# Kernel tuning notes

Hardware: AMD Instinct MI355X
Metric: run time of the kernel (lower is better)

The kernel has to match this reference:

```python
import jax, jax.numpy as jnp
import numpy as np
from jax import lax

B = 128

# ---- 4-qubit statevector helpers (RY + CNOT circuit is real-valued) ----

def _init_state(n):
    s = jnp.zeros((n, 2, 2, 2, 2), jnp.float32)
    return s.at[:, 0, 0, 0, 0].set(1.0)


def _ry(state, theta, wire):
    # RY(t) = [[cos t/2, -sin t/2],[sin t/2, cos t/2]]; theta: scalar or [N]
    s = jnp.moveaxis(state, wire + 1, 1)
    c = jnp.cos(theta * 0.5)
    sn = jnp.sin(theta * 0.5)
    if jnp.ndim(theta) > 0:
        c = c.reshape(-1, 1, 1, 1)
        sn = sn.reshape(-1, 1, 1, 1)
    a, b = s[:, 0], s[:, 1]
    s = jnp.stack([c * a - sn * b, sn * a + c * b], axis=1)
    return jnp.moveaxis(s, 1, wire + 1)


def _cnot(state, ctrl, tgt):
    s = jnp.moveaxis(state, [ctrl + 1, tgt + 1], [1, 2])
    s = jnp.concatenate([s[:, :1], jnp.flip(s[:, 1:], axis=2)], axis=1)
    return jnp.moveaxis(s, [1, 2], [ctrl + 1, tgt + 1])


def _random_layer(state, thetas):
    for i in range(4):
        state = _ry(state, thetas[i], i)
        state = _cnot(state, i, (i + 1) % 4)
    return state


def _measure_z(state, wire):
    p = jnp.moveaxis(state, wire + 1, 1) ** 2
    p = p.reshape(p.shape[0], 2, -1).sum(-1)
    return p[:, 0] - p[:, 1]


def setup_inputs() -> dict:
    key = jax.random.key(0)
    ks = jax.random.split(key, 12)

    def n(k, shape, scale):
        return jax.random.normal(k, shape, jnp.float32) * scale

    return {
        "x": jax.random.normal(ks[0], (B, 3, 249, 249), jnp.float32),
        "conv1_w": n(ks[1], (6, 3, 5, 5), 0.1),
        "conv1_b": jnp.zeros((6,), jnp.float32),
        "conv2_w": n(ks[2], (15, 6, 3, 3), 0.1),
        "conv2_b": jnp.zeros((15,), jnp.float32),
        "fc1_w": n(ks[3], (120, 55815), 1.0 / np.sqrt(55815.0)),
        "fc1_b": jnp.zeros((120,), jnp.float32),
        "fc2_w": n(ks[4], (84, 120), 1.0 / np.sqrt(120.0)),
        "fc2_b": jnp.zeros((84,), jnp.float32),
        "fc3_w": n(ks[5], (1, 84), 1.0 / np.sqrt(84.0)),
        "fc3_b": jnp.zeros((1,), jnp.float32),
        "head_thetas": jax.random.uniform(ks[6], (4,), jnp.float32, 0.0, 2.0 * np.pi),
        "qf_thetas": jax.random.uniform(ks[7], (4,), jnp.float32, 0.0, 2.0 * np.pi),
        "lin_w": n(ks[8], (1, 784), 1.0 / np.sqrt(784.0)),
        "lin_b": jnp.zeros((1,), jnp.float32),
    }


def reference(x, conv1_w, conv1_b, conv2_w, conv2_b, fc1_w, fc1_b, fc2_w, fc2_b,
              fc3_w, fc3_b, head_thetas, qf_thetas, lin_w, lin_b):
    bsz = x.shape[0]

    def conv(y, w, b, stride):
        y = lax.conv_general_dilated(y, w, (stride, stride), [(1, 1), (1, 1)],
                                     dimension_numbers=("NCHW", "OIHW", "NCHW"))
        return y + b[None, :, None, None]

    def pool(y):  # MaxPool2d(kernel=2, stride=1)
        return lax.reduce_window(y, -jnp.inf, lax.max, (1, 1, 2, 2), (1, 1, 1, 1), "VALID")

    # ---- conv branch (dropout = identity in eval) ----
    h = pool(jax.nn.relu(conv(x, conv1_w, conv1_b, 2)))          # [B,6,123,123]
    h = pool(jax.nn.relu(conv(h, conv2_w, conv2_b, 2)))          # [B,15,61,61]
    h = h.reshape(bsz, -1)                                        # [B,55815]
    h = jax.nn.relu(h @ fc1_w.T + fc1_b)
    h = jax.nn.relu(h @ fc2_w.T + fc2_b)
    logit = (h @ fc3_w.T + fc3_b)[:, 0]                           # [B]
    st = _init_state(bsz)
    st = _ry(st, logit, 0)
    st = _random_layer(st, head_thetas)
    probs_conv = jax.nn.sigmoid(_measure_z(st, 0))[:, None]       # [B,1]

    # ---- quanvolution branch ----
    gray = x.mean(axis=1, keepdims=True)                          # [B,1,249,249]
    g = jax.image.resize(gray, (bsz, 1, 28, 28), method="linear")[:, 0]
    # 2x2 patches, row-major, element order [tl, tr, bl, br]
    patches = g.reshape(bsz, 14, 2, 14, 2).transpose(0, 1, 3, 2, 4).reshape(bsz * 196, 4)
    st = _init_state(bsz * 196)
    for w in range(4):
        st = _ry(st, patches[:, w], w)
    st = _random_layer(st, qf_thetas)
    feats = jnp.stack([_measure_z(st, w) for w in range(4)], axis=1).reshape(bsz, 784)
    probs_q = jax.nn.sigmoid(feats @ lin_w.T + lin_b)             # [B,1]

    probs = (probs_conv + probs_q) * 0.5
    return jnp.concatenate([probs, 1.0 - probs], axis=-1)         # [B,2]
```

## Files before the change

### kernel.cpp

```cpp
#include <hip/hip_runtime.h>
#include <math.h>

#define DEV static __device__ __forceinline__

template <int W>
DEV void q_ry(float s[16], float th) {
  float c = cosf(th * 0.5f), sn = sinf(th * 0.5f);
  constexpr int m = 8 >> W;
#pragma unroll
  for (int i = 0; i < 16; ++i) {
    if (!(i & m)) {
      float a = s[i], b = s[i | m];
      s[i] = c * a - sn * b;
      s[i | m] = sn * a + c * b;
    }
  }
}
template <int C, int T>
DEV void q_cnot(float s[16]) {
  constexpr int mc = 8 >> C, mt = 8 >> T;
#pragma unroll
  for (int i = 0; i < 16; ++i) {
    if ((i & mc) && !(i & mt)) {
      float t = s[i]; s[i] = s[i | mt]; s[i | mt] = t;
    }
  }
}
template <int W>
DEV float q_mz(const float s[16]) {
  constexpr int m = 8 >> W;
  float p = 0.f;
#pragma unroll
  for (int i = 0; i < 16; ++i) p += (i & m) ? -s[i] * s[i] : s[i] * s[i];
  return p;
}
DEV void q_layer(float s[16], const float* __restrict__ th) {
  q_ry<0>(s, th[0]); q_cnot<0, 1>(s);
  q_ry<1>(s, th[1]); q_cnot<1, 2>(s);
  q_ry<2>(s, th[2]); q_cnot<2, 3>(s);
  q_ry<3>(s, th[3]); q_cnot<3, 0>(s);
}

__global__ void k_wre(const float* __restrict__ c1w, float* __restrict__ wre1) {
  int t = blockIdx.x * 256 + threadIdx.x;
  if (t < 450) {
    int g = t / 30, rem = t % 30;
    int ci = g / 5, ky = g % 5, kx = rem / 6, co = rem % 6;
    wre1[t] = c1w[co * 75 + ci * 25 + ky * 5 + kx];
  }
}

DEV int c1_rowbase(int row) { return row * 39 + ((row >> 1) & 1); }

__global__ __launch_bounds__(256, 4) void k_conv1(const float* __restrict__ x,
                                                  const float* __restrict__ wre1,
                                                  const float* __restrict__ bia,
                                                  float* __restrict__ out) {
  __shared__ float smem[6800];
  float (*ct)[42][19] = (float (*)[42][19])smem;
  int b = blockIdx.z;
  int PY0 = blockIdx.y * 41, PX0 = blockIdx.x * 16;
  int iy0 = PY0 * 2 - 1, ix0 = PX0 * 2 - 1;
  int tid = threadIdx.x;
  const float* xb = x + (size_t)b * 186003;
  int r = tid / 6, seg = tid - 6 * (tid / 6);
  float acc[6][3];
#pragma unroll
  for (int co = 0; co < 6; ++co) {
    float bv = bia[co];
#pragma unroll
    for (int c = 0; c < 3; ++c) acc[co][c] = bv;
  }
  {
    const float* xci = xb;
#pragma unroll
    for (int s = 0; s < 14; ++s) {
      int idx = s * 256 + tid;
      bool ok = idx < 3393;
      int rr = idx / 39, cc = idx - rr * 39;
      int iy = iy0 + rr, ix = ix0 + cc;
      float v = 0.f;
      if (ok && cc < 37 && (unsigned)iy < 249u && (unsigned)ix < 249u)
        v = xci[iy * 249 + ix];
      if (ok && cc < 37) smem[c1_rowbase(rr) + cc] = v;
    }
  }
  __syncthreads();
#pragma unroll
  for (int ci = 0; ci < 3; ++ci) {
    float vreg[14];
    if (ci < 2) {
      const float* xci = xb + (ci + 1) * 62001;
#pragma unroll
      for (int s = 0; s < 14; ++s) {
        int idx = s * 256 + tid;
        bool ok = idx < 3393;
        int rr = idx / 39, cc = idx - rr * 39;
        int iy = iy0 + rr, ix = ix0 + cc;
        float v = 0.f;
        if (ok && cc < 37 && (unsigned)iy < 249u && (unsigned)ix < 249u)
          v = xci[iy * 249 + ix];
        vreg[s] = v;
      }
    }
    const float* buf = smem + (ci & 1) * 3400;
    if (tid < 252) {
#pragma unroll
      for (int ky = 0; ky < 5; ++ky) {
        const float* xrow = &buf[c1_rowbase(2 * r + ky) + 6 * seg];
        float xv[10];
#pragma unroll
        for (int j = 0; j < 10; ++j) xv[j] = xrow[j];
        const float* wp = wre1 + (ci * 5 + ky) * 30;
        float wr[30];
#pragma unroll
        for (int j = 0; j < 30; ++j) wr[j] = wp[j];
#pragma unroll
        for (int c = 0; c < 3; ++c)
#pragma unroll
          for (int kx = 0; kx < 5; ++kx)
#pragma unroll
            for (int co = 0; co < 6; ++co)
              acc[co][c] += xv[2 * c + kx] * wr[kx * 6 + co];
      }
    }
    if (ci < 2) {
      float* nbuf = smem + ((ci + 1) & 1) * 3400;
#pragma unroll
      for (int s = 0; s < 14; ++s) {
        int idx = s * 256 + tid;
        bool ok = idx < 3393;
        int rr = idx / 39, cc = idx - rr * 39;
        if (ok && cc < 37) nbuf[c1_rowbase(rr) + cc] = vreg[s];
      }
    }
    __syncthreads();
  }
  if (tid < 252) {
#pragma unroll
    for (int co = 0; co < 6; ++co)
#pragma unroll
      for (int c = 0; c < 3; ++c)
        if (3 * seg + c < 17) ct[co][r][3 * seg + c] = acc[co][c];
  }
  __syncthreads();
#pragma unroll
  for (int co2 = 0; co2 < 6; ++co2) {
    for (int j = tid; j < 41 * 16; j += 256) {
      int pr = j >> 4, pc = j & 15;
      float m = fmaxf(fmaxf(ct[co2][pr][pc], ct[co2][pr][pc + 1]),
                      fmaxf(ct[co2][pr + 1][pc], ct[co2][pr + 1][pc + 1]));
      out[((size_t)(b * 6 + co2) * 123 + PY0 + pr) * 128 + PX0 + pc] = fmaxf(m, 0.f);
    }
  }
}

__global__ __launch_bounds__(256, 4) void k_conv2(const float* __restrict__ in,
                                                  const float* __restrict__ w,
                                                  const float* __restrict__ bia,
                                                  float* __restrict__ out) {
  __shared__ float smem[6 * 35 * 36];
  float (*xs)[35][36] = (float (*)[35][36])smem;
  float (*ct)[17][18] = (float (*)[17][18])smem;
  int b = blockIdx.z;
  int py0 = blockIdx.y * 16, px0 = blockIdx.x * 16;
  int iy0 = py0 * 2 - 1, ix0 = px0 * 2 - 1;
  int tid = threadIdx.x;
  const float* ib = in + (size_t)b * 94464;
  for (int idx = tid; idx < 6 * 35 * 36; idx += 256) {
    int ci = idx / 1260, rem = idx % 1260, rr = rem / 36, cc = rem % 36;
    int iy = iy0 + rr, ix = ix0 + cc;
    float v = 0.f;
    if (cc < 35 && (unsigned)iy < 123u && (unsigned)ix < 123u)
      v = ib[ci * 15744 + iy * 128 + ix];
    xs[ci][rr][cc] = v;
  }
  __syncthreads();
  int co = tid % 15, ty = tid / 15;
  float acc[17];
  if (tid < 255) {
    float bv = bia[co];
#pragma unroll
    for (int t = 0; t < 17; ++t) acc[t] = bv;
#pragma unroll
    for (int ci = 0; ci < 6; ++ci) {
      float wreg[9];
#pragma unroll
      for (int j = 0; j < 9; ++j) wreg[j] = w[co * 54 + ci * 9 + j];
#pragma unroll
      for (int ky = 0; ky < 3; ++ky) {
        const float* xrow = &xs[ci][2 * ty + ky][0];
        float xv[36];
#pragma unroll
        for (int j = 0; j < 18; ++j) {
          float2 t2 = *reinterpret_cast<const float2*>(&xrow[2 * j]);
          xv[2 * j] = t2.x; xv[2 * j + 1] = t2.y;
        }
#pragma unroll
        for (int tx = 0; tx < 17; ++tx)
#pragma unroll
          for (int kx = 0; kx < 3; ++kx)
            acc[tx] += xv[2 * tx + kx] * wreg[ky * 3 + kx];
      }
    }
  }
  __syncthreads();
  if (tid < 255) {
#pragma unroll
    for (int tx = 0; tx < 17; ++tx) ct[co][ty][tx] = acc[tx];
  }
  __syncthreads();
  for (int i = tid; i < 15 * 16 * 16; i += 256) {
    int co2 = i / 256, rem = i % 256, pr = rem / 16, pc = rem % 16;
    int py = py0 + pr, px = px0 + pc;
    if (py < 61 && px < 61) {
      float m = fmaxf(fmaxf(ct[co2][pr][pc], ct[co2][pr][pc + 1]),
                      fmaxf(ct[co2][pr + 1][pc], ct[co2][pr + 1][pc + 1]));
      out[(size_t)b * 55815 + co2 * 3721 + py * 61 + px] = fmaxf(m, 0.f);
    }
  }
}

#define KFC 55815
#define NCHUNK 1745
#define FC1_BLOCKS 512
__global__ __launch_bounds__(256) void k_fc1(const float* __restrict__ h,
                                             const float* __restrict__ w,
                                             float* __restrict__ partial) {
  __shared__ float hs[128][33];
  __shared__ float wsd[120][33];
  int tid = threadIdx.x;
  int tb = tid & 31;
  int bo = tid >> 5;
  float acc[4][15];
#pragma unroll
  for (int j = 0; j < 4; ++j)
#pragma unroll
    for (int oo = 0; oo < 15; ++oo) acc[j][oo] = 0.f;

  for (int ch = blockIdx.x; ch < NCHUNK; ch += FC1_BLOCKS) {
    int k0 = ch * 32;
    for (int idx = tid; idx < 128 * 32; idx += 256) {
      int bb = idx >> 5, kk = idx & 31;
      int k = k0 + kk;
      hs[bb][kk] = (k < KFC) ? h[(size_t)bb * KFC + k] : 0.f;
    }
    for (int idx = tid; idx < 120 * 32; idx += 256) {
      int oo = idx >> 5, kk = idx & 31;
      int k = k0 + kk;
      wsd[oo][kk] = (k < KFC) ? w[(size_t)oo * KFC + k] : 0.f;
    }
    __syncthreads();
#pragma unroll 4
    for (int kk = 0; kk < 32; ++kk) {
      float hv[4], wv[15];
#pragma unroll
      for (int j = 0; j < 4; ++j) hv[j] = hs[tb + 32 * j][kk];
#pragma unroll
      for (int oo = 0; oo < 15; ++oo) wv[oo] = wsd[bo * 15 + oo][kk];
#pragma unroll
      for (int j = 0; j < 4; ++j)
#pragma unroll
        for (int oo = 0; oo < 15; ++oo) acc[j][oo] += hv[j] * wv[oo];
    }
    __syncthreads();
  }
  float* pg = partial + (size_t)blockIdx.x * 15360;
#pragma unroll
  for (int j = 0; j < 4; ++j) {
    int b = tb + 32 * j;
#pragma unroll
    for (int oo = 0; oo < 15; ++oo) pg[b * 120 + bo * 15 + oo] = acc[j][oo];
  }
}

__global__ __launch_bounds__(256) void k_reduceA(const float* __restrict__ partial,
                                                 float* __restrict__ partial2) {
  int gs = blockIdx.x / 60;
  int blk = blockIdx.x % 60;
  int i = blk * 256 + threadIdx.x;
  float a = 0.f;
#pragma unroll 8
  for (int g = gs * 32; g < gs * 32 + 32; ++g)
    a += partial[(size_t)g * 15360 + i];
  partial2[(size_t)gs * 15360 + i] = a;
}

__global__ __launch_bounds__(256) void k_reduceB(const float* __restrict__ partial2,
                                                 const float* __restrict__ bias,
                                                 float* __restrict__ outv) {
  int i = blockIdx.x * 256 + threadIdx.x;
  float a = bias[i % 120];
#pragma unroll
  for (int gs = 0; gs < 16; ++gs) a += partial2[(size_t)gs * 15360 + i];
  outv[i] = fmaxf(a, 0.f);
}

__global__ __launch_bounds__(128) void k_head(const float* __restrict__ fc1o,
                                              const float* __restrict__ w2,
                                              const float* __restrict__ b2,
                                              const float* __restrict__ w3,
                                              const float* __restrict__ b3,
                                              const float* __restrict__ hth,
                                              float* __restrict__ probs_conv) {
  __shared__ float h1[120];
  __shared__ float h2[84];
  int b = blockIdx.x, tid = threadIdx.x;
  if (tid < 120) h1[tid] = fc1o[b * 120 + tid];
  __syncthreads();
  if (tid < 84) {
    float a = b2[tid];
    for (int k = 0; k < 120; ++k) a += h1[k] * w2[tid * 120 + k];
    h2[tid] = fmaxf(a, 0.f);
  }
  __syncthreads();
  if (tid == 0) {
    float lg = b3[0];
    for (int j = 0; j < 84; ++j) lg += h2[j] * w3[j];
    float s[16];
#pragma unroll
    for (int i = 0; i < 16; ++i) s[i] = 0.f;
    s[0] = 1.f;
    q_ry<0>(s, lg);
    q_layer(s, hth);
    float z = q_mz<0>(s);
    probs_conv[b] = 1.f / (1.f + expf(-z));
  }
}

DEV void resize_win(int o, int& i0, int& i1, float& sf, float& inorm) {
  const float invs = 249.0f / 28.0f;
  sf = ((float)o + 0.5f) * invs - 0.5f;
  i0 = (int)ceilf(sf - invs); if (i0 < 0) i0 = 0;
  i1 = (int)floorf(sf + invs); if (i1 > 248) i1 = 248;
  float nrm = 0.f;
  for (int i = i0; i <= i1; ++i)
    nrm += fmaxf(0.f, 1.f - fabsf(sf - (float)i) * (28.0f / 249.0f));
  inorm = 1.f / nrm;
}

__global__ __launch_bounds__(256) void k_resize1(const float* __restrict__ x,
                                                 float* __restrict__ tmp) {
  __shared__ float accs[8][28][32];
  __shared__ float sf_t[28], inorm_t[28];
  int b = blockIdx.x >> 3, cg = blockIdx.x & 7;
  int tid = threadIdx.x;
  int iysub = tid >> 5, lane = tid & 31;
  int col = cg * 32 + lane;
  bool colok = col < 249;
  for (int i = tid; i < 8 * 28 * 32; i += 256) ((float*)accs)[i] = 0.f;
  if (tid < 28) {
    int i0, i1; float sf, inm;
    resize_win(tid, i0, i1, sf, inm);
    sf_t[tid] = sf; inorm_t[tid] = inm;
  }
  __syncthreads();
  const float* xb = x + (size_t)b * 186003;
  const float S = 28.0f / 249.0f;
  for (int it = 0; it < 32; ++it) {
    int iy = it * 8 + iysub;
    if (iy < 249 && colok) {
      int off = iy * 249 + col;
      float gray = (xb[off] + xb[62001 + off] + xb[124002 + off]) * (1.0f / 3.0f);
      float u = ((float)iy + 0.5f) * S;
      int oyh = (int)floorf(u + 0.5f);
#pragma unroll
      for (int d = 0; d < 2; ++d) {
        int oy = oyh - d;
        if (oy >= 0 && oy < 28) {
          float wv = fmaxf(0.f, 1.f - fabsf(sf_t[oy] - (float)iy) * S) * inorm_t[oy];
          accs[iysub][oy][lane] += wv * gray;
        }
      }
    }
  }
  __syncthreads();
  for (int i = tid; i < 28 * 32; i += 256) {
    int oy = i >> 5, c2 = i & 31;
    int colw = cg * 32 + c2;
    if (colw < 249) {
      float a = 0.f;
#pragma unroll
      for (int u2 = 0; u2 < 8; ++u2) a += accs[u2][oy][c2];
      tmp[((size_t)b * 28 + oy) * 249 + colw] = a;
    }
  }
}

__global__ __launch_bounds__(256) void k_quanv(const float* __restrict__ tmp,
                                               const float* __restrict__ qth,
                                               const float* __restrict__ lw,
                                               float* __restrict__ qpart) {
  __shared__ float g[392];
  __shared__ float red[4];
  int bid = blockIdx.x;
  int b = bid >> 1, half = bid & 1;
  int tid = threadIdx.x;
  for (int idx = tid; idx < 392; idx += 256) {
    int ly = idx / 28, ox = idx % 28;
    int oy = 14 * half + ly;
    int i0, i1; float sf, inorm;
    resize_win(ox, i0, i1, sf, inorm);
    const float* tr = tmp + ((size_t)b * 28 + oy) * 249;
    float acc = 0.f;
    for (int i = i0; i <= i1; ++i)
      acc += fmaxf(0.f, 1.f - fabsf(sf - (float)i) * (28.0f / 249.0f)) * inorm * tr[i];
    g[idx] = acc;
  }
  __syncthreads();
  float part = 0.f;
  if (tid < 98) {
    int pl = tid / 14, pj = tid % 14;
    int pi = 7 * half + pl;
    float v0 = g[(2 * pl) * 28 + 2 * pj];
    float v1 = g[(2 * pl) * 28 + 2 * pj + 1];
    float v2 = g[(2 * pl + 1) * 28 + 2 * pj];
    float v3 = g[(2 * pl + 1) * 28 + 2 * pj + 1];
    float s[16];
#pragma unroll
    for (int i = 0; i < 16; ++i) s[i] = 0.f;
    s[0] = 1.f;
    q_ry<0>(s, v0); q_ry<1>(s, v1); q_ry<2>(s, v2); q_ry<3>(s, v3);
    q_layer(s, qth);
    float z0 = q_mz<0>(s), z1 = q_mz<1>(s), z2 = q_mz<2>(s), z3 = q_mz<3>(s);
    const float* lwp = lw + (pi * 14 + pj) * 4;
    part = z0 * lwp[0] + z1 * lwp[1] + z2 * lwp[2] + z3 * lwp[3];
  }
#pragma unroll
  for (int off = 32; off > 0; off >>= 1) part += __shfl_down(part, off, 64);
  if ((tid & 63) == 0) red[tid >> 6] = part;
  __syncthreads();
  if (tid == 0) qpart[bid] = red[0] + red[1] + red[2] + red[3];
}

__global__ __launch_bounds__(128) void k_final(const float* __restrict__ qpart,
                                               const float* __restrict__ lb,
                                               const float* __restrict__ probs_conv,
                                               float* __restrict__ out) {
  int b = threadIdx.x;
  float tot = qpart[2 * b] + qpart[2 * b + 1] + lb[0];
  float pq = 1.f / (1.f + expf(-tot));
  float pr = 0.5f * (probs_conv[b] + pq);
  out[b * 2 + 0] = pr;
  out[b * 2 + 1] = 1.f - pr;
}

extern "C" void kernel_launch(void* const* d_in, const int* in_sizes, int n_in,
                              void* d_out, int out_size, void* d_ws, size_t ws_size,
                              hipStream_t stream) {
  const float* x   = (const float*)d_in[0];
  const float* c1w = (const float*)d_in[1];
  const float* c1b = (const float*)d_in[2];
  const float* c2w = (const float*)d_in[3];
  const float* c2b = (const float*)d_in[4];
  const float* f1w = (const float*)d_in[5];
  const float* f1b = (const float*)d_in[6];
  const float* f2w = (const float*)d_in[7];
  const float* f2b = (const float*)d_in[8];
  const float* f3w = (const float*)d_in[9];
  const float* f3b = (const float*)d_in[10];
  const float* hth = (const float*)d_in[11];
  const float* qth = (const float*)d_in[12];
  const float* lw  = (const float*)d_in[13];
  const float* lb  = (const float*)d_in[14];
  float* out = (float*)d_out;
  char* ws = (char*)d_ws;

  float* pool1    = (float*)(ws);
  float* partial  = (float*)(ws);
  float* tmp      = (float*)(ws + 33554432);
  float* h        = (float*)(ws + 48365568);
  float* fc1o     = (float*)(ws + 76942848);
  float* pconv    = (float*)(ws + 77004288);
  float* wre1     = (float*)(ws + 77004800);
  float* qpart    = (float*)(ws + 77009848);
  float* partial2 = (float*)(ws + 77012992);

  k_wre<<<dim3(2), 256, 0, stream>>>(c1w, wre1);
  k_conv1<<<dim3(8, 3, 128), 256, 0, stream>>>(x, wre1, c1b, pool1);
  k_conv2<<<dim3(4, 4, 128), 256, 0, stream>>>(pool1, c2w, c2b, h);
  k_fc1<<<dim3(FC1_BLOCKS), 256, 0, stream>>>(h, f1w, partial);
  k_reduceA<<<dim3(960), 256, 0, stream>>>(partial, partial2);
  k_reduceB<<<dim3(60), 256, 0, stream>>>(partial2, f1b, fc1o);
  k_head<<<dim3(128), 128, 0, stream>>>(fc1o, f2w, f2b, f3w, f3b, hth, pconv);
  k_resize1<<<dim3(1024), 256, 0, stream>>>(x, tmp);
  k_quanv<<<dim3(256), 256, 0, stream>>>(tmp, qth, lw, qpart);
  k_final<<<dim3(1), 128, 0, stream>>>(qpart, lb, pconv, out);
}
```

Before: 271.1 us.

## Replace double-buffered conv1 input staging with single buffer and rolled channel loop

Removes the register-prefetch double-buffering of input channels in conv1. Each channel is now loaded directly into a single shared buffer inside a non-unrolled loop, with extra barriers between load and compute. This cuts LDS use from 6800 to 4800 floats and drops the 14-register prefetch array, aiming for higher occupancy and less register pressure. In exchange it gives up overlap of global loads with compute and adds synchronisation per channel.

```diff
diff --git a/kernel.cpp b/kernel.cpp
--- a/kernel.cpp
+++ b/kernel.cpp
@@ -56,7 +56,7 @@
                                                   const float* __restrict__ wre1,
                                                   const float* __restrict__ bia,
                                                   float* __restrict__ out) {
-  __shared__ float smem[6800];
+  __shared__ float smem[4800];
   float (*ct)[42][19] = (float (*)[42][19])smem;
   int b = blockIdx.z;
   int PY0 = blockIdx.y * 41, PX0 = blockIdx.x * 16;
@@ -71,8 +71,10 @@
 #pragma unroll
     for (int c = 0; c < 3; ++c) acc[co][c] = bv;
   }
-  {
-    const float* xci = xb;
+#pragma unroll 1
+  for (int ci = 0; ci < 3; ++ci) {
+    if (ci) __syncthreads();
+    const float* xci = xb + ci * 62001;
 #pragma unroll
     for (int s = 0; s < 14; ++s) {
       int idx = s * 256 + tid;
@@ -84,30 +86,11 @@
         v = xci[iy * 249 + ix];
       if (ok && cc < 37) smem[c1_rowbase(rr) + cc] = v;
     }
-  }
-  __syncthreads();
-#pragma unroll
-  for (int ci = 0; ci < 3; ++ci) {
-    float vreg[14];
-    if (ci < 2) {
-      const float* xci = xb + (ci + 1) * 62001;
-#pragma unroll
-      for (int s = 0; s < 14; ++s) {
-        int idx = s * 256 + tid;
-        bool ok = idx < 3393;
-        int rr = idx / 39, cc = idx - rr * 39;
-        int iy = iy0 + rr, ix = ix0 + cc;
-        float v = 0.f;
-        if (ok && cc < 37 && (unsigned)iy < 249u && (unsigned)ix < 249u)
-          v = xci[iy * 249 + ix];
-        vreg[s] = v;
-      }
-    }
-    const float* buf = smem + (ci & 1) * 3400;
+    __syncthreads();
     if (tid < 252) {
 #pragma unroll
       for (int ky = 0; ky < 5; ++ky) {
-        const float* xrow = &buf[c1_rowbase(2 * r + ky) + 6 * seg];
+        const float* xrow = &smem[c1_rowbase(2 * r + ky) + 6 * seg];
         float xv[10];
 #pragma unroll
         for (int j = 0; j < 10; ++j) xv[j] = xrow[j];
@@ -124,18 +107,8 @@
               acc[co][c] += xv[2 * c + kx] * wr[kx * 6 + co];
       }
     }
-    if (ci < 2) {
-      float* nbuf = smem + ((ci + 1) & 1) * 3400;
-#pragma unroll
-      for (int s = 0; s < 14; ++s) {
-        int idx = s * 256 + tid;
-        bool ok = idx < 3393;
-        int rr = idx / 39, cc = idx - rr * 39;
-        if (ok && cc < 37) nbuf[c1_rowbase(rr) + cc] = vreg[s];
-      }
-    }
-    __syncthreads();
-  }
+  }
+  __syncthreads();
   if (tid < 252) {
 #pragma unroll
     for (int co = 0; co < 6; ++co)
```

Result: faster. 248.5 us (-8.4%).
